# Optimization experiments

Measured on AMD Instinct MI355X. Metric: run time of the kernel, lower is better.

## Reference

```python
import jax, jax.numpy as jnp
import numpy as np

B, N, C, H = 8, 1024, 256, 8   # graphs, nodes per graph, channels, heads
E = 131072                      # edges (avg degree 16)
DK = C // H
EPS = 1e-5


def setup_inputs() -> dict:
    key = jax.random.key(0)
    ks = jax.random.split(key, 16)
    s = 1.0 / np.sqrt(C)
    d = {
        'x': jax.random.normal(ks[0], (B * N, C), jnp.float32),
        'edge_index': jax.random.randint(ks[1], (2, E), 0, B * N, dtype=jnp.int64),
        'sph': jax.random.uniform(ks[2], (B, 1, N, N), jnp.float32),
        # local conv (GraphConv-style): root + neighbor linear
        'Wr': jax.random.normal(ks[3], (C, C), jnp.float32) * s,
        'Wn': jax.random.normal(ks[4], (C, C), jnp.float32) * s,
        # attention in/out projections (4 Linears as in MultiheadAttention)
        'Wq': jax.random.normal(ks[5], (C, C), jnp.float32) * s,
        'bq': jnp.zeros((C,), jnp.float32),
        'Wk': jax.random.normal(ks[6], (C, C), jnp.float32) * s,
        'bk': jnp.zeros((C,), jnp.float32),
        'Wv': jax.random.normal(ks[7], (C, C), jnp.float32) * s,
        'bv': jnp.zeros((C,), jnp.float32),
        'Wo': jax.random.normal(ks[8], (C, C), jnp.float32) * s,
        'bo': jnp.zeros((C,), jnp.float32),
        # MLP: C -> 2C -> C
        'W1': jax.random.normal(ks[9], (C, 2 * C), jnp.float32) * s,
        'b1': jnp.zeros((2 * C,), jnp.float32),
        'W2': jax.random.normal(ks[10], (2 * C, C), jnp.float32) * (1.0 / np.sqrt(2 * C)),
        'b2': jnp.zeros((C,), jnp.float32),
        # three batch norms (affine)
        'gamma1': jnp.ones((C,), jnp.float32), 'beta1': jnp.zeros((C,), jnp.float32),
        'gamma2': jnp.ones((C,), jnp.float32), 'beta2': jnp.zeros((C,), jnp.float32),
        'gamma3': jnp.ones((C,), jnp.float32), 'beta3': jnp.zeros((C,), jnp.float32),
    }
    return d


def _bn(h, g, b):
    # BatchNorm1d (training mode): per-feature stats over all nodes
    m = h.mean(axis=0)
    v = h.var(axis=0)
    return (h - m) * jax.lax.rsqrt(v + EPS) * g + b


def reference(x, edge_index, sph, Wr, Wn, Wq, bq, Wk, bk, Wv, bv, Wo, bo,
              W1, b1, W2, b2, gamma1, beta1, gamma2, beta2, gamma3, beta3):
    src, dst = edge_index[0], edge_index[1]

    # 1) local MPNN branch: h = conv(x) + x, then norm1
    msg = (x @ Wn)[src]                                   # [E, C]
    agg = jax.ops.segment_sum(msg, dst, num_segments=B * N)
    h1 = _bn(x @ Wr + agg + x, gamma1, beta1)             # [BN, C]

    # 2) global sph-modulated attention branch (dense batch is a reshape:
    #    equal-size graphs -> mask all True)
    hd = x.reshape(B, N, C)
    q = (hd @ Wq + bq).reshape(B, N, H, DK).transpose(0, 2, 1, 3)  # [B,H,N,DK]
    k = (hd @ Wk + bk).reshape(B, N, H, DK).transpose(0, 2, 1, 3)
    v = (hd @ Wv + bv).reshape(B, N, H, DK).transpose(0, 2, 1, 3)
    scores = jnp.einsum('bhnd,bhmd->bhnm', q, k) * (1.0 / np.sqrt(DK))
    scores = scores * sph                                  # structural modulation
    p = jax.nn.softmax(scores, axis=-1)
    o = jnp.einsum('bhnm,bhmd->bhnd', p, v)                # [B,H,N,DK]
    o = o.transpose(0, 2, 1, 3).reshape(B * N, C) @ Wo + bo
    h2 = _bn(o + x, gamma2, beta2)

    # 3) sum branches, MLP residual, norm3
    out = h1 + h2
    out = out + (jax.nn.relu(out @ W1 + b1) @ W2 + b2)
    return _bn(out, gamma3, beta3)
```

## Files before the change

### kernel.cpp

```cpp
#include <hip/hip_runtime.h>
#include <hip/hip_bf16.h>

constexpr int Bg  = 8;
constexpr int Nn  = 1024;
constexpr int Cc  = 256;
constexpr int Hh  = 8;
constexpr int DKh = 32;
constexpr int Ee  = 131072;
constexpr int BNn = Bg * Nn;
#define EPSV 1e-5f


typedef __attribute__((ext_vector_type(8))) short bf16x8;
typedef __attribute__((ext_vector_type(4))) float f32x4;

static __device__ __forceinline__ unsigned short f2b(float v) {
    __hip_bfloat16 h = __float2bfloat16(v);
    return __builtin_bit_cast(unsigned short, h);
}
static __device__ __forceinline__ float b2f(unsigned short u) {
    unsigned int x = ((unsigned int)u) << 16;
    return __builtin_bit_cast(float, x);
}
static __device__ __forceinline__ bf16x8 ldb8(const unsigned short* p) {
    return *(const bf16x8*)p;
}

__global__ __launch_bounds__(256) void prep_k(
    const float* __restrict__ x, unsigned short* __restrict__ xf,
    unsigned short* __restrict__ xlo,
    const float* __restrict__ Wr, const float* __restrict__ Wn,
    const float* __restrict__ Wq, const float* __restrict__ Wk,
    const float* __restrict__ Wv, const float* __restrict__ Wo,
    const float* __restrict__ W1, const float* __restrict__ W2,
    unsigned short* __restrict__ WcatT,
    unsigned short* __restrict__ WqT, unsigned short* __restrict__ WkT,
    unsigned short* __restrict__ WvT, unsigned short* __restrict__ WoT,
    unsigned short* __restrict__ W1T, unsigned short* __restrict__ W2T,
    const int* __restrict__ ei, int* __restrict__ deg)
{
    int blk = blockIdx.x;
    if (blk < 2048) {
        int i = (blk * 256 + threadIdx.x) * 4;
        float4 v = *(const float4*)(x + i);
        int r = i >> 8, c = i & 255;
        ushort4 pk;
        pk.x = f2b(v.x); pk.y = f2b(v.y); pk.z = f2b(v.z); pk.w = f2b(v.w);
        *(ushort4*)(xlo + (size_t)r * 256 + c) = pk;
        *(ushort4*)(xf + ((size_t)(r >> 4) * 16 + (c >> 5)) * 512
                    + (r & 15) * 32 + (c & 31)) = pk;
    } else if (blk < 4608) {
        int idx = (blk - 2048) * 256 + threadIdx.x;
        if (idx < 131072) {
            int n = idx >> 9, k = idx & 511;
            float v = (k < 256) ? Wr[k * 256 + n] : Wn[(k - 256) * 256 + n];
            WcatT[((size_t)(n >> 4) * 16 + (k >> 5)) * 512 + (n & 15) * 32 + (k & 31)] = f2b(v);
        } else if (idx < 393216) {
            int l = idx - 131072;
            int wsel = l >> 16; l &= 65535;
            int n = l >> 8, kk = l & 255;
            const float* S = wsel == 0 ? Wq : wsel == 1 ? Wk : wsel == 2 ? Wv : Wo;
            unsigned short* D = wsel == 0 ? WqT : wsel == 1 ? WkT : wsel == 2 ? WvT : WoT;
            D[((size_t)(n >> 4) * 8 + (kk >> 5)) * 512 + (n & 15) * 32 + (kk & 31)]
                = f2b(S[kk * 256 + n]);
        } else if (idx < 524288) {
            int l = idx - 393216;
            int n = l >> 8, kk = l & 255;
            W1T[((size_t)(n >> 4) * 8 + (kk >> 5)) * 512 + (n & 15) * 32 + (kk & 31)]
                = f2b(W1[kk * 512 + n]);
        } else {
            int l = idx - 524288;
            int n = l >> 9, kk = l & 511;
            W2T[((size_t)(n >> 4) * 16 + (kk >> 5)) * 512 + (n & 15) * 32 + (kk & 31)]
                = f2b(W2[kk * 256 + n]);
        }
    } else {
        int e = (blk - 4608) * 256 + threadIdx.x;
        atomicAdd(&deg[ei[Ee + e]], 1);
    }
}

__global__ __launch_bounds__(256) void scan_k(
    const int* __restrict__ deg, int* __restrict__ rowst, int* __restrict__ cursor)
{
    __shared__ int partial[256];
    int t = threadIdx.x;
    int local[32];
    int s = 0;
    #pragma unroll
    for (int i = 0; i < 32; ++i) { local[i] = deg[i * 256 + t]; s += local[i]; }
    partial[t] = s;
    __syncthreads();
    for (int off = 1; off < 256; off <<= 1) {
        int v = (t >= off) ? partial[t - off] : 0;
        __syncthreads();
        partial[t] += v;
        __syncthreads();
    }
    int base = partial[t] - s;
    #pragma unroll
    for (int i = 0; i < 32; ++i) {
        int n = i * 256 + t;
        rowst[n] = base;
        cursor[n] = base;
        base += local[i];
    }
}

__global__ __launch_bounds__(256) void place_k(
    const int* __restrict__ ei, int* __restrict__ cursor, int* __restrict__ eidx)
{
    int e = blockIdx.x * 256 + threadIdx.x;
    int s = ei[e], d = ei[Ee + e];
    int pos = atomicAdd(&cursor[d], 1);
    eidx[pos] = s;
}

__global__ __launch_bounds__(256, 4) void gather_qkv_k(
    const unsigned short* __restrict__ xlo, const int* __restrict__ rowst,
    const int* __restrict__ deg, const int* __restrict__ eidx,
    unsigned short* __restrict__ xf,
    const unsigned short* __restrict__ WT,
    const float* __restrict__ bq, const float* __restrict__ bk,
    const float* __restrict__ bv,
    unsigned short* __restrict__ qb, unsigned short* __restrict__ kb,
    unsigned short* __restrict__ vTb, float qscale)
{
    __shared__ unsigned short vtile[64][40];
    int blk = blockIdx.x;

    if (blk < 2048) {
        int n = blk * 4 + (threadIdx.x >> 6);
        int c4 = (threadIdx.x & 63) * 4;
        int b0 = rowst[n], d = deg[n];
        float4 acc = {0.f, 0.f, 0.f, 0.f};
        int i = 0;
        for (; i + 4 <= d; i += 4) {
            int s0 = eidx[b0 + i], s1 = eidx[b0 + i + 1];
            int s2 = eidx[b0 + i + 2], s3 = eidx[b0 + i + 3];
            ushort4 a0 = *(const ushort4*)(xlo + (size_t)s0 * 256 + c4);
            ushort4 a1 = *(const ushort4*)(xlo + (size_t)s1 * 256 + c4);
            ushort4 a2 = *(const ushort4*)(xlo + (size_t)s2 * 256 + c4);
            ushort4 a3 = *(const ushort4*)(xlo + (size_t)s3 * 256 + c4);
            acc.x += (b2f(a0.x) + b2f(a1.x)) + (b2f(a2.x) + b2f(a3.x));
            acc.y += (b2f(a0.y) + b2f(a1.y)) + (b2f(a2.y) + b2f(a3.y));
            acc.z += (b2f(a0.z) + b2f(a1.z)) + (b2f(a2.z) + b2f(a3.z));
            acc.w += (b2f(a0.w) + b2f(a1.w)) + (b2f(a2.w) + b2f(a3.w));
        }
        for (; i < d; ++i) {
            int s = eidx[b0 + i];
            ushort4 a = *(const ushort4*)(xlo + (size_t)s * 256 + c4);
            acc.x += b2f(a.x); acc.y += b2f(a.y);
            acc.z += b2f(a.z); acc.w += b2f(a.w);
        }
        ushort4 pk;
        pk.x = f2b(acc.x); pk.y = f2b(acc.y); pk.z = f2b(acc.z); pk.w = f2b(acc.w);
        int cg2 = 256 + c4;
        *(ushort4*)(xf + ((size_t)(n >> 4) * 16 + (cg2 >> 5)) * 512
                    + (n & 15) * 32 + (cg2 & 31)) = pk;
        return;
    }

    int qblk = blk - 2048;
    const int n0 = (qblk % 12) * 64;
    const int m0 = (qblk / 12) * 32;
    const int t = threadIdx.x;
    const int wave = t >> 6, lane = t & 63;
    const int tl = lane & 15, g = lane >> 4;
    const int wr = wave >> 1, wc = wave & 1;
    const int which = n0 >> 8;

    f32x4 acc[2] = {};

    const unsigned short* a0 = xf + (size_t)((m0 >> 4) + wr) * 16 * 512 + tl * 32 + g * 8;
    const unsigned short* b0 = WT + ((size_t)(n0 >> 4) + wc * 2) * 8 * 512 + tl * 32 + g * 8;
    const unsigned short* b1 = b0 + 8 * 512;

    for (int k0 = 0; k0 < 256; k0 += 32) {
        bf16x8 af  = ldb8(a0 + (k0 >> 5) * 512);
        bf16x8 bf0 = ldb8(b0 + (k0 >> 5) * 512), bf1 = ldb8(b1 + (k0 >> 5) * 512);
        acc[0] = __builtin_amdgcn_mfma_f32_16x16x32_bf16(af, bf0, acc[0], 0, 0, 0);
        acc[1] = __builtin_amdgcn_mfma_f32_16x16x32_bf16(af, bf1, acc[1], 0, 0, 0);
    }

    const float* bias = which == 0 ? bq : which == 1 ? bk : bv;
    const float sc = which == 0 ? qscale : 1.f;

    if (which == 0) {
        #pragma unroll
        for (int c16 = 0; c16 < 2; ++c16)
            #pragma unroll
            for (int reg = 0; reg < 4; ++reg) {
                int row = m0 + wr * 16 + g * 4 + reg;
                int col = (n0 & 255) + wc * 32 + c16 * 16 + tl;
                qb[(size_t)row * Cc + col] = f2b((acc[c16][reg] + bias[col]) * sc);
            }
    } else if (which == 1) {
        #pragma unroll
        for (int c16 = 0; c16 < 2; ++c16)
            #pragma unroll
            for (int reg = 0; reg < 4; ++reg) {
                int row = m0 + wr * 16 + g * 4 + reg;
                int col = (n0 & 255) + wc * 32 + c16 * 16 + tl;
                kb[((size_t)(row >> 4) * 8 + (col >> 5)) * 512
                   + (row & 15) * 32 + (col & 31)] = f2b(acc[c16][reg] + bias[col]);
            }
    } else {
        #pragma unroll
        for (int c16 = 0; c16 < 2; ++c16)
            #pragma unroll
            for (int reg = 0; reg < 4; ++reg) {
                int colL = wc * 32 + c16 * 16 + tl;
                int rowL = wr * 16 + g * 4 + reg;
                vtile[colL][rowL] = f2b(acc[c16][reg] + bias[(n0 & 255) + colL]);
            }
        __syncthreads();
        int clocal = t >> 2, q4 = t & 3;
        int colg = (n0 & 255) + clocal;
        int hh = colg >> 5, dd = colg & 31;
        int bg = m0 >> 10;
        int m_loc = (m0 & 1023) + q4 * 8;
        int mt64 = m_loc >> 6, ks = (m_loc >> 5) & 1, gg = (m_loc >> 3) & 3;
        int cg = dd >> 4, tlv = dd & 15;
        ushort4 u0 = *(ushort4*)&vtile[clocal][q4 * 8];
        ushort4 u1 = *(ushort4*)&vtile[clocal][q4 * 8 + 4];
        unsigned short* dst = vTb
            + (((size_t)(bg * Hh + hh) * 16 + mt64) * 2048)
            + ((size_t)((ks * 2 + cg) * 16 + tlv) * 32) + gg * 8;
        *(ushort4*)dst = u0;
        *(ushort4*)(dst + 4) = u1;
    }
}

__global__ __launch_bounds__(512, 8) void attn_h1_k(
    const unsigned short* __restrict__ q, const unsigned short* __restrict__ k,
    const unsigned short* __restrict__ vT, const float* __restrict__ sph,
    unsigned short* __restrict__ op0,
    const unsigned short* __restrict__ xf, const unsigned short* __restrict__ WcatT,
    const float* __restrict__ x, unsigned short* __restrict__ h1preb,
    float* __restrict__ gsum, float* __restrict__ gsq)
{
    __shared__ float Sph[2][16][132];
    __shared__ unsigned short Ps[Hh][16][72];
    float* csum = (float*)&Ps[0][0][0];
    float* csq  = csum + 256;

    const int blk = blockIdx.x;
    const int t = threadIdx.x;
    const int wave = t >> 6;
    const int lane = t & 63;
    const int tl = lane & 15, g = lane >> 4;

    if (blk < 512) {
        const int b  = blk & 7;
        const int n0 = (blk >> 3) * 16;
        const int w  = wave;

        bf16x8 qf = ldb8(q + ((size_t)(b * Nn + n0 + tl)) * Cc + w * DKh + g * 8);

        float lsum = 0.f;
        f32x4 oacc[2] = {};

        const unsigned short* kfb = k + ((size_t)(b * 512 + w)) * 512 + tl * 32 + g * 8;
        const unsigned short* vfb = vT + ((size_t)(b * Hh + w) * 16) * 2048
                                     + (size_t)tl * 32 + g * 8;
        const float* sbase = sph + ((size_t)b * Nn + n0) * Nn;

        if (t < 256) {
            int r1 = t >> 4, c1 = (t & 15) * 8;
            const float* src = sbase + (size_t)r1 * Nn + c1;
            *(float4*)&Sph[0][r1][c1]     = *(const float4*)src;
            *(float4*)&Sph[0][r1][c1 + 4] = *(const float4*)(src + 4);
        }
        __syncthreads();

        int cur = 0;
        for (int it = 0; it < 8; ++it) {
            const int m0 = it * 128;
            if (it < 7 && t < 256) {
                int r1 = t >> 4, c1 = (t & 15) * 8;
                const float* src = sbase + (size_t)r1 * Nn + m0 + 128 + c1;
                *(float4*)&Sph[cur ^ 1][r1][c1]     = *(const float4*)src;
                *(float4*)&Sph[cur ^ 1][r1][c1 + 4] = *(const float4*)(src + 4);
            }

            #pragma unroll
            for (int half = 0; half < 2; ++half) {
                const int mh = m0 + half * 64;

                f32x4 st[4];
                #pragma unroll
                for (int mg = 0; mg < 4; ++mg) {
                    bf16x8 ka = ldb8(kfb + (size_t)((mh >> 4) + mg) * 4096);
                    f32x4 z = {0.f, 0.f, 0.f, 0.f};
                    st[mg] = __builtin_amdgcn_mfma_f32_16x16x32_bf16(ka, qf, z, 0, 0, 0);
                }

                #pragma unroll
                for (int mg = 0; mg < 4; ++mg) {
                    float4 sp = *(const float4*)&Sph[cur][tl][half * 64 + mg * 16 + g * 4];
                    float p0 = __builtin_amdgcn_exp2f(st[mg][0] * sp.x);
                    float p1 = __builtin_amdgcn_exp2f(st[mg][1] * sp.y);
                    float p2 = __builtin_amdgcn_exp2f(st[mg][2] * sp.z);
                    float p3 = __builtin_amdgcn_exp2f(st[mg][3] * sp.w);
                    lsum += (p0 + p1) + (p2 + p3);
                    ushort4 pk;
                    pk.x = f2b(p0); pk.y = f2b(p1); pk.z = f2b(p2); pk.w = f2b(p3);
                    *(ushort4*)&Ps[w][tl][mg * 16 + g * 4] = pk;
                }

                const unsigned short* vtile64 = vfb + (size_t)(mh >> 6) * 2048;
                #pragma unroll
                for (int ks = 0; ks < 2; ++ks) {
                    bf16x8 pa = ldb8(&Ps[w][tl][ks * 32 + g * 8]);
                    #pragma unroll
                    for (int cg = 0; cg < 2; ++cg) {
                        bf16x8 vb = ldb8(vtile64 + (size_t)(ks * 2 + cg) * 512);
                        oacc[cg] = __builtin_amdgcn_mfma_f32_16x16x32_bf16(pa, vb, oacc[cg], 0, 0, 0);
                    }
                }
            }

            __syncthreads();
            cur ^= 1;
        }

        lsum += __shfl_xor(lsum, 16);
        lsum += __shfl_xor(lsum, 32);
        float* shl = (float*)&Ps[w][0][0];
        if (g == 0) shl[tl] = lsum;
        const size_t rt = (size_t)((b * Nn + n0) >> 4);
        #pragma unroll
        for (int r = 0; r < 4; ++r) {
            float inv = 1.f / shl[g * 4 + r];
            #pragma unroll
            for (int cg = 0; cg < 2; ++cg)
                op0[(rt * 8 + w) * 512 + (g * 4 + r) * 32 + cg * 16 + tl]
                    = f2b(oacc[cg][r] * inv);
        }
        return;
    }

    const int wrg = wave >> 2;
    const int wcg = wave & 3;
    const int m0g = (blk - 512) * 32;
    const int N = Cc;

    if (t < 256) { csum[t] = 0.f; csq[t] = 0.f; }
    __syncthreads();

    f32x4 acc[4] = {};

    const unsigned short* a0 = xf + (size_t)((m0g >> 4) + wrg) * 16 * 512 + tl * 32 + g * 8;
    const unsigned short* bb = WcatT + (size_t)(wcg * 4) * 16 * 512 + tl * 32 + g * 8;

    for (int k0 = 0; k0 < 512; k0 += 32) {
        bf16x8 af = ldb8(a0 + (k0 >> 5) * 512);
        #pragma unroll
        for (int c16 = 0; c16 < 4; ++c16) {
            bf16x8 bf = ldb8(bb + ((size_t)c16 * 16 + (k0 >> 5)) * 512);
            acc[c16] = __builtin_amdgcn_mfma_f32_16x16x32_bf16(af, bf, acc[c16], 0, 0, 0);
        }
    }

    #pragma unroll
    for (int c16 = 0; c16 < 4; ++c16) {
        int col = wcg * 64 + c16 * 16 + tl;
        float ls = 0.f, lq = 0.f;
        #pragma unroll
        for (int reg = 0; reg < 4; ++reg) {
            int row = m0g + wrg * 16 + g * 4 + reg;
            size_t idx = (size_t)row * N + col;
            float v = acc[c16][reg] + x[idx];
            ls += v; lq += v * v;
            h1preb[idx] = f2b(v);
        }
        atomicAdd(&csum[col], ls);
        atomicAdd(&csq[col],  lq);
    }
    __syncthreads();
    if (t < 256) {
        atomicAdd(&gsum[t], csum[t]);
        atomicAdd(&gsq[t],  csq[t]);
    }
}

__global__ __launch_bounds__(256, 4) void mlp1_k(
    const unsigned short* __restrict__ A,
    const unsigned short* __restrict__ WT,
    const float* __restrict__ bias,
    unsigned short* __restrict__ outb)
{
    const int t = threadIdx.x;
    const int wave = t >> 6, lane = t & 63;
    const int tl = lane & 15, g = lane >> 4;
    const int wr = wave >> 1, wc = wave & 1;
    const int m0 = blockIdx.y * 32, n0 = blockIdx.x * 64;

    f32x4 acc[2] = {};

    const unsigned short* a0 = A  + (size_t)((m0 >> 4) + wr) * 8 * 512 + tl * 32 + g * 8;
    const unsigned short* b0 = WT + ((size_t)(n0 >> 4) + wc * 2) * 8 * 512 + tl * 32 + g * 8;
    const unsigned short* b1 = b0 + 8 * 512;

    for (int k0 = 0; k0 < 256; k0 += 32) {
        bf16x8 af  = ldb8(a0 + (k0 >> 5) * 512);
        bf16x8 bf0 = ldb8(b0 + (k0 >> 5) * 512), bf1 = ldb8(b1 + (k0 >> 5) * 512);
        acc[0] = __builtin_amdgcn_mfma_f32_16x16x32_bf16(af, bf0, acc[0], 0, 0, 0);
        acc[1] = __builtin_amdgcn_mfma_f32_16x16x32_bf16(af, bf1, acc[1], 0, 0, 0);
    }

    const size_t rtO = (size_t)(m0 >> 4) + wr;
    #pragma unroll
    for (int c16 = 0; c16 < 2; ++c16) {
        int col  = n0 + wc * 32 + c16 * 16 + tl;
        int ktO  = col >> 5;
        #pragma unroll
        for (int reg = 0; reg < 4; ++reg) {
            float v = fmaxf(acc[c16][reg] + bias[col], 0.f);
            outb[(rtO * 16 + ktO) * 512 + (g * 4 + reg) * 32 + (col & 31)] = f2b(v);
        }
    }
}

__global__ __launch_bounds__(256, 4) void mlp2_k(
    const unsigned short* __restrict__ A,
    const unsigned short* __restrict__ WT,
    const float* __restrict__ bias,
    const unsigned short* __restrict__ addb,
    float* __restrict__ outf,
    float* __restrict__ gsum, float* __restrict__ gsq)
{
    const int N = Cc;
    const int t = threadIdx.x;
    const int wave = t >> 6, lane = t & 63;
    const int tl = lane & 15, g = lane >> 4;
    const int wr = wave >> 1, wc = wave & 1;
    const int m0 = blockIdx.y * 32, n0 = blockIdx.x * 64;

    __shared__ float csum[64], csq[64];
    if (t < 64) { csum[t] = 0.f; csq[t] = 0.f; }
    __syncthreads();

    f32x4 acc[2] = {};

    const unsigned short* a0 = A  + (size_t)((m0 >> 4) + wr) * 16 * 512 + tl * 32 + g * 8;
    const unsigned short* b0 = WT + ((size_t)(n0 >> 4) + wc * 2) * 16 * 512 + tl * 32 + g * 8;
    const unsigned short* b1 = b0 + 16 * 512;

    for (int k0 = 0; k0 < 512; k0 += 32) {
        bf16x8 af  = ldb8(a0 + (k0 >> 5) * 512);
        bf16x8 bf0 = ldb8(b0 + (k0 >> 5) * 512), bf1 = ldb8(b1 + (k0 >> 5) * 512);
        acc[0] = __builtin_amdgcn_mfma_f32_16x16x32_bf16(af, bf0, acc[0], 0, 0, 0);
        acc[1] = __builtin_amdgcn_mfma_f32_16x16x32_bf16(af, bf1, acc[1], 0, 0, 0);
    }

    const size_t rtR = (size_t)(m0 >> 4) + wr;
    #pragma unroll
    for (int c16 = 0; c16 < 2; ++c16) {
        int colL = wc * 32 + c16 * 16 + tl;
        int col  = n0 + colL;
        int ktR  = col >> 5;
        float ls = 0.f, lq = 0.f;
        #pragma unroll
        for (int reg = 0; reg < 4; ++reg) {
            int row = m0 + wr * 16 + g * 4 + reg;
            float v = acc[c16][reg] + bias[col]
                    + b2f(addb[(rtR * 8 + ktR) * 512 + (g * 4 + reg) * 32 + (col & 31)]);
            ls += v; lq += v * v;
            outf[(size_t)row * N + col] = v;
        }
        atomicAdd(&csum[colL], ls); atomicAdd(&csq[colL], lq);
    }
    __syncthreads();
    if (t < 64) {
        atomicAdd(&gsum[n0 + t], csum[t]);
        atomicAdd(&gsq[n0 + t],  csq[t]);
    }
}

__global__ __launch_bounds__(256, 4) void gemm_attnA_k(
    const unsigned short* __restrict__ op0,
    const unsigned short* __restrict__ WT, const float* __restrict__ bias,
    const float* __restrict__ add1, unsigned short* __restrict__ h2preb,
    float* __restrict__ gsum, float* __restrict__ gsq)
{
    const int N = Cc;
    const int t = threadIdx.x;
    const int wave = t >> 6, lane = t & 63;
    const int tl = lane & 15, g = lane >> 4;
    const int wr = wave >> 1, wc = wave & 1;
    const int m0 = blockIdx.y * 32, n0 = blockIdx.x * 64;

    __shared__ float csum[64], csq[64];
    if (t < 64) { csum[t] = 0.f; csq[t] = 0.f; }
    __syncthreads();

    f32x4 acc[2] = {};

    const unsigned short* a0b = op0 + (size_t)((m0 >> 4) + wr) * 8 * 512 + tl * 32 + g * 8;
    const unsigned short* b0 = WT + ((size_t)(n0 >> 4) + wc * 2) * 8 * 512 + tl * 32 + g * 8;
    const unsigned short* b1 = b0 + 8 * 512;

    for (int k0 = 0; k0 < 256; k0 += 32) {
        bf16x8 af  = ldb8(a0b + (k0 >> 5) * 512);
        bf16x8 bf0 = ldb8(b0 + (k0 >> 5) * 512), bf1 = ldb8(b1 + (k0 >> 5) * 512);
        acc[0] = __builtin_amdgcn_mfma_f32_16x16x32_bf16(af, bf0, acc[0], 0, 0, 0);
        acc[1] = __builtin_amdgcn_mfma_f32_16x16x32_bf16(af, bf1, acc[1], 0, 0, 0);
    }

    #pragma unroll
    for (int c16 = 0; c16 < 2; ++c16) {
        int colL = wc * 32 + c16 * 16 + tl;
        int col  = n0 + colL;
        float ls = 0.f, lq = 0.f;
        #pragma unroll
        for (int reg = 0; reg < 4; ++reg) {
            int row = m0 + wr * 16 + g * 4 + reg;
            float v = acc[c16][reg] + bias[col];
            size_t idx = (size_t)row * N + col;
            v += add1[idx];
            ls += v; lq += v * v;
            h2preb[idx] = f2b(v);
        }
        atomicAdd(&csum[colL], ls); atomicAdd(&csq[colL], lq);
    }
    __syncthreads();
    if (t < 64) {
        atomicAdd(&gsum[n0 + t], csum[t]);
        atomicAdd(&gsq[n0 + t],  csq[t]);
    }
}

__global__ __launch_bounds__(256) void bn_apply_k(
    const float* __restrict__ h, const float* __restrict__ gsum,
    const float* __restrict__ gsq, const float* __restrict__ gamma,
    const float* __restrict__ beta, float* __restrict__ outf)
{
    size_t i4 = ((size_t)blockIdx.x * 256 + threadIdx.x) * 4;
    int ch = (int)(i4 & (Cc - 1));
    float4 hv = *(const float4*)(h + i4);
    float4 sm = *(const float4*)(gsum + ch);
    float4 sq = *(const float4*)(gsq + ch);
    float4 ga = *(const float4*)(gamma + ch);
    float4 be = *(const float4*)(beta + ch);
    float4 o;
    {
        float m = sm.x * (1.f / BNn), var = sq.x * (1.f / BNn) - m * m;
        o.x = (hv.x - m) * rsqrtf(var + EPSV) * ga.x + be.x;
    }
    {
        float m = sm.y * (1.f / BNn), var = sq.y * (1.f / BNn) - m * m;
        o.y = (hv.y - m) * rsqrtf(var + EPSV) * ga.y + be.y;
    }
    {
        float m = sm.z * (1.f / BNn), var = sq.z * (1.f / BNn) - m * m;
        o.z = (hv.z - m) * rsqrtf(var + EPSV) * ga.z + be.z;
    }
    {
        float m = sm.w * (1.f / BNn), var = sq.w * (1.f / BNn) - m * m;
        o.w = (hv.w - m) * rsqrtf(var + EPSV) * ga.w + be.w;
    }
    *(float4*)(outf + i4) = o;
}

__global__ __launch_bounds__(256) void bn_apply12_k(
    const unsigned short* __restrict__ h1preb, const unsigned short* __restrict__ h2preb,
    const float* __restrict__ stats,
    const float* __restrict__ g1, const float* __restrict__ be1,
    const float* __restrict__ g2, const float* __restrict__ be2,
    unsigned short* __restrict__ outb)
{
    size_t i4 = ((size_t)blockIdx.x * 256 + threadIdx.x) * 4;
    int ch = (int)(i4 & (Cc - 1));
    ushort4 u1 = *(const ushort4*)(h1preb + i4);
    ushort4 u2 = *(const ushort4*)(h2preb + i4);
    float4 s1m = *(const float4*)(stats + ch);
    float4 s1q = *(const float4*)(stats + 256 + ch);
    float4 s2m = *(const float4*)(stats + 512 + ch);
    float4 s2q = *(const float4*)(stats + 768 + ch);
    float4 G1 = *(const float4*)(g1 + ch),  B1 = *(const float4*)(be1 + ch);
    float4 G2 = *(const float4*)(g2 + ch),  B2 = *(const float4*)(be2 + ch);
    ushort4 pk;
    #define BN12C(comp, ucomp) { \
        float m1 = s1m.comp * (1.f / BNn), v1 = s1q.comp * (1.f / BNn) - m1 * m1; \
        float m2 = s2m.comp * (1.f / BNn), v2 = s2q.comp * (1.f / BNn) - m2 * m2; \
        float o = (b2f(u1.ucomp) - m1) * rsqrtf(v1 + EPSV) * G1.comp + B1.comp \
                + (b2f(u2.ucomp) - m2) * rsqrtf(v2 + EPSV) * G2.comp + B2.comp; \
        pk.ucomp = f2b(o); }
    BN12C(x, x) BN12C(y, y) BN12C(z, z) BN12C(w, w)
    #undef BN12C
    int row = (int)(i4 >> 8), col = ch;
    *(ushort4*)(outb + ((size_t)(row >> 4) * 8 + (col >> 5)) * 512
                + (row & 15) * 32 + (col & 31)) = pk;
}

extern "C" void kernel_launch(void* const* d_in, const int* in_sizes, int n_in,
                              void* d_out, int out_size, void* d_ws, size_t ws_size,
                              hipStream_t stream)
{
    const float* x   = (const float*)d_in[0];
    const int*   ei  = (const int*)  d_in[1];
    const float* sph = (const float*)d_in[2];
    const float* Wr  = (const float*)d_in[3];
    const float* Wn  = (const float*)d_in[4];
    const float* Wq  = (const float*)d_in[5];
    const float* bq  = (const float*)d_in[6];
    const float* Wk  = (const float*)d_in[7];
    const float* bk  = (const float*)d_in[8];
    const float* Wv  = (const float*)d_in[9];
    const float* bv  = (const float*)d_in[10];
    const float* Wo  = (const float*)d_in[11];
    const float* bo  = (const float*)d_in[12];
    const float* W1  = (const float*)d_in[13];
    const float* b1  = (const float*)d_in[14];
    const float* W2  = (const float*)d_in[15];
    const float* b2  = (const float*)d_in[16];
    const float* g1  = (const float*)d_in[17];
    const float* be1 = (const float*)d_in[18];
    const float* g2  = (const float*)d_in[19];
    const float* be2 = (const float*)d_in[20];
    const float* g3  = (const float*)d_in[21];
    const float* be3 = (const float*)d_in[22];
    float* out = (float*)d_out;

    const size_t SL = (size_t)BNn * Cc;

    float* ws = (float*)d_ws;
    float* s1 = ws;
    float* s2 = s1 + SL;
    float* s3 = s2 + SL;

    int*   deg      = (int*)(s3 + SL);
    float* statsAll = (float*)(deg + 8192);
    int*   rowst    = (int*)(statsAll + 1536);
    int*   cursor   = rowst + 8256;
    int*   eidx     = cursor + 8192;

    unsigned short* xf  = (unsigned short*)(eidx + 131072);
    unsigned short* qb  = xf + 2 * SL;
    unsigned short* kb  = qb + SL;
    unsigned short* vTb = kb + SL;
    unsigned short* osb = kb;
    unsigned short* hid = xf;

    unsigned short* WcatT = vTb + SL;
    unsigned short* WqT   = WcatT + 131072;
    unsigned short* WkT   = WqT + 65536;
    unsigned short* WvT   = WkT + 65536;
    unsigned short* WoT   = WvT + 65536;
    unsigned short* W1T   = WoT + 65536;
    unsigned short* W2T   = W1T + 131072;
    unsigned short* xlo   = W2T + 131072;
    unsigned short* op0b   = (unsigned short*)s1;
    unsigned short* h1preb = (unsigned short*)s2;
    unsigned short* h2preb = (unsigned short*)s3;

    dim3 gN256(4, 256);
    dim3 gN512(8, 256);

    const float QSCALE = 0.17677669529663687f * 1.4426950408889634f;

    hipMemsetAsync(deg, 0, (8192 + 1536) * sizeof(float), stream);
    prep_k<<<5120, 256, 0, stream>>>(x, xf, xlo, Wr, Wn, Wq, Wk, Wv, Wo, W1, W2,
                                     WcatT, WqT, WkT, WvT, WoT, W1T, W2T, ei, deg);
    scan_k<<<1, 256, 0, stream>>>(deg, rowst, cursor);
    place_k<<<Ee / 256, 256, 0, stream>>>(ei, cursor, eidx);
    gather_qkv_k<<<5120, 256, 0, stream>>>(xlo, rowst, deg, eidx, xf,
                                           WqT, bq, bk, bv, qb, kb, vTb, QSCALE);
    attn_h1_k<<<768, 512, 0, stream>>>(qb, kb, vTb, sph, op0b,
                                       xf, WcatT, x, h1preb,
                                       statsAll, statsAll + 256);
    gemm_attnA_k<<<gN256, 256, 0, stream>>>(op0b, WoT, bo, x,
                                            h2preb, statsAll + 512, statsAll + 768);
    bn_apply12_k<<<(int)(SL / 1024), 256, 0, stream>>>(h1preb, h2preb, statsAll,
                                                       g1, be1, g2, be2, osb);
    mlp1_k<<<gN512, 256, 0, stream>>>(osb, W1T, b1, hid);
    mlp2_k<<<gN256, 256, 0, stream>>>(hid, W2T, b2, osb, s2,
                                      statsAll + 1024, statsAll + 1280);
    bn_apply_k<<<(int)(SL / 1024), 256, 0, stream>>>(s2, statsAll + 1024,
                                                     statsAll + 1280, g3, be3, out);
}
```

Baseline: 282.9 us.

## Process two query row tiles per attention block to reuse K/V loads

Measured after the change: 322.9 us. 1.14x slower.

```diff
diff --git a/kernel.cpp b/kernel.cpp
--- a/kernel.cpp
+++ b/kernel.cpp
@@ -232,7 +232,7 @@
     }
 }
 
-__global__ __launch_bounds__(512, 8) void attn_h1_k(
+__global__ __launch_bounds__(512, 6) void attn_h1_k(
     const unsigned short* __restrict__ q, const unsigned short* __restrict__ k,
     const unsigned short* __restrict__ vT, const float* __restrict__ sph,
     unsigned short* __restrict__ op0,
@@ -240,7 +240,7 @@
     const float* __restrict__ x, unsigned short* __restrict__ h1preb,
     float* __restrict__ gsum, float* __restrict__ gsq)
 {
-    __shared__ float Sph[2][16][132];
+    __shared__ float Sph[2][32][132];
     __shared__ unsigned short Ps[Hh][16][72];
     float* csum = (float*)&Ps[0][0][0];
     float* csq  = csum + 256;
@@ -251,22 +251,25 @@
     const int lane = t & 63;
     const int tl = lane & 15, g = lane >> 4;
 
-    if (blk < 512) {
+    if (blk < 256) {
         const int b  = blk & 7;
-        const int n0 = (blk >> 3) * 16;
+        const int n0 = (blk >> 3) * 32;
         const int w  = wave;
 
-        bf16x8 qf = ldb8(q + ((size_t)(b * Nn + n0 + tl)) * Cc + w * DKh + g * 8);
-
-        float lsum = 0.f;
-        f32x4 oacc[2] = {};
+        bf16x8 qf[2];
+        #pragma unroll
+        for (int qs = 0; qs < 2; ++qs)
+            qf[qs] = ldb8(q + ((size_t)(b * Nn + n0 + qs * 16 + tl)) * Cc + w * DKh + g * 8);
+
+        float lsum[2] = {0.f, 0.f};
+        f32x4 oacc[2][2] = {};
 
         const unsigned short* kfb = k + ((size_t)(b * 512 + w)) * 512 + tl * 32 + g * 8;
         const unsigned short* vfb = vT + ((size_t)(b * Hh + w) * 16) * 2048
                                      + (size_t)tl * 32 + g * 8;
         const float* sbase = sph + ((size_t)b * Nn + n0) * Nn;
 
-        if (t < 256) {
+        {
             int r1 = t >> 4, c1 = (t & 15) * 8;
             const float* src = sbase + (size_t)r1 * Nn + c1;
             *(float4*)&Sph[0][r1][c1]     = *(const float4*)src;
@@ -277,7 +280,7 @@
         int cur = 0;
         for (int it = 0; it < 8; ++it) {
             const int m0 = it * 128;
-            if (it < 7 && t < 256) {
+            if (it < 7) {
                 int r1 = t >> 4, c1 = (t & 15) * 8;
                 const float* src = sbase + (size_t)r1 * Nn + m0 + 128 + c1;
                 *(float4*)&Sph[cur ^ 1][r1][c1]     = *(const float4*)src;
@@ -288,35 +291,48 @@
             for (int half = 0; half < 2; ++half) {
                 const int mh = m0 + half * 64;
 
-                f32x4 st[4];
+                bf16x8 ka[4];
                 #pragma unroll
-                for (int mg = 0; mg < 4; ++mg) {
-                    bf16x8 ka = ldb8(kfb + (size_t)((mh >> 4) + mg) * 4096);
-                    f32x4 z = {0.f, 0.f, 0.f, 0.f};
-                    st[mg] = __builtin_amdgcn_mfma_f32_16x16x32_bf16(ka, qf, z, 0, 0, 0);
-                }
-
+                for (int mg = 0; mg < 4; ++mg)
+                    ka[mg] = ldb8(kfb + (size_t)((mh >> 4) + mg) * 4096);
+                const unsigned short* vtile64 = vfb + (size_t)(mh >> 6) * 2048;
+                bf16x8 vb[2][2];
                 #pragma unroll
-                for (int mg = 0; mg < 4; ++mg) {
-                    float4 sp = *(const float4*)&Sph[cur][tl][half * 64 + mg * 16 + g * 4];
-                    float p0 = __builtin_amdgcn_exp2f(st[mg][0] * sp.x);
-                    float p1 = __builtin_amdgcn_exp2f(st[mg][1] * sp.y);
-                    float p2 = __builtin_amdgcn_exp2f(st[mg][2] * sp.z);
-                    float p3 = __builtin_amdgcn_exp2f(st[mg][3] * sp.w);
-                    lsum += (p0 + p1) + (p2 + p3);
-                    ushort4 pk;
-                    pk.x = f2b(p0); pk.y = f2b(p1); pk.z = f2b(p2); pk.w = f2b(p3);
-                    *(ushort4*)&Ps[w][tl][mg * 16 + g * 4] = pk;
-                }
-
-                const unsigned short* vtile64 = vfb + (size_t)(mh >> 6) * 2048;
+                for (int ks = 0; ks < 2; ++ks)
+                    #pragma unroll
+                    for (int cg = 0; cg < 2; ++cg)
+                        vb[ks][cg] = ldb8(vtile64 + (size_t)(half * 2 * 0 + ks * 2 + cg) * 512);
+
                 #pragma unroll
-                for (int ks = 0; ks < 2; ++ks) {
-                    bf16x8 pa = ldb8(&Ps[w][tl][ks * 32 + g * 8]);
+                for (int qs = 0; qs < 2; ++qs) {
+                    f32x4 st[4];
                     #pragma unroll
-                    for (int cg = 0; cg < 2; ++cg) {
-                        bf16x8 vb = ldb8(vtile64 + (size_t)(ks * 2 + cg) * 512);
-                        oacc[cg] = __builtin_amdgcn_mfma_f32_16x16x32_bf16(pa, vb, oacc[cg], 0, 0, 0);
+                    for (int mg = 0; mg < 4; ++mg) {
+                        f32x4 z = {0.f, 0.f, 0.f, 0.f};
+                        st[mg] = __builtin_amdgcn_mfma_f32_16x16x32_bf16(ka[mg], qf[qs], z, 0, 0, 0);
+                    }
+
+                    #pragma unroll
+                    for (int mg = 0; mg < 4; ++mg) {
+                        float4 sp = *(const float4*)&Sph[cur][qs * 16 + tl]
+                                        [half * 64 + mg * 16 + g * 4];
+                        float p0 = __builtin_amdgcn_exp2f(st[mg][0] * sp.x);
+                        float p1 = __builtin_amdgcn_exp2f(st[mg][1] * sp.y);
+                        float p2 = __builtin_amdgcn_exp2f(st[mg][2] * sp.z);
+                        float p3 = __builtin_amdgcn_exp2f(st[mg][3] * sp.w);
+                        lsum[qs] += (p0 + p1) + (p2 + p3);
+                        ushort4 pk;
+                        pk.x = f2b(p0); pk.y = f2b(p1); pk.z = f2b(p2); pk.w = f2b(p3);
+                        *(ushort4*)&Ps[w][tl][mg * 16 + g * 4] = pk;
+                    }
+
+                    #pragma unroll
+                    for (int ks = 0; ks < 2; ++ks) {
+                        bf16x8 pa = ldb8(&Ps[w][tl][ks * 32 + g * 8]);
+                        #pragma unroll
+                        for (int cg = 0; cg < 2; ++cg)
+                            oacc[qs][cg] = __builtin_amdgcn_mfma_f32_16x16x32_bf16(
+                                pa, vb[ks][cg], oacc[qs][cg], 0, 0, 0);
                     }
                 }
             }
@@ -325,25 +341,31 @@
             cur ^= 1;
         }
 
-        lsum += __shfl_xor(lsum, 16);
-        lsum += __shfl_xor(lsum, 32);
         float* shl = (float*)&Ps[w][0][0];
-        if (g == 0) shl[tl] = lsum;
-        const size_t rt = (size_t)((b * Nn + n0) >> 4);
-        #pragma unroll
-        for (int r = 0; r < 4; ++r) {
-            float inv = 1.f / shl[g * 4 + r];
+        #pragma unroll
+        for (int qs = 0; qs < 2; ++qs) {
+            float ls = lsum[qs];
+            ls += __shfl_xor(ls, 16);
+            ls += __shfl_xor(ls, 32);
+            if (g == 0) shl[qs * 16 + tl] = ls;
+        }
+        const size_t rt0 = (size_t)((b * Nn + n0) >> 4);
+        #pragma unroll
+        for (int qs = 0; qs < 2; ++qs)
             #pragma unroll
-            for (int cg = 0; cg < 2; ++cg)
-                op0[(rt * 8 + w) * 512 + (g * 4 + r) * 32 + cg * 16 + tl]
-                    = f2b(oacc[cg][r] * inv);
-        }
+            for (int r = 0; r < 4; ++r) {
+                float inv = 1.f / shl[qs * 16 + g * 4 + r];
+                #pragma unroll
+                for (int cg = 0; cg < 2; ++cg)
+                    op0[((rt0 + qs) * 8 + w) * 512 + (g * 4 + r) * 32 + cg * 16 + tl]
+                        = f2b(oacc[qs][cg][r] * inv);
+            }
         return;
     }
 
     const int wrg = wave >> 2;
     const int wcg = wave & 3;
-    const int m0g = (blk - 512) * 32;
+    const int m0g = (blk - 256) * 32;
     const int N = Cc;
 
     if (t < 256) { csum[t] = 0.f; csq[t] = 0.f; }
@@ -668,7 +690,7 @@
     place_k<<<Ee / 256, 256, 0, stream>>>(ei, cursor, eidx);
     gather_qkv_k<<<5120, 256, 0, stream>>>(xlo, rowst, deg, eidx, xf,
                                            WqT, bq, bk, bv, qb, kb, vTb, QSCALE);
-    attn_h1_k<<<768, 512, 0, stream>>>(qb, kb, vTb, sph, op0b,
+    attn_h1_k<<<512, 512, 0, stream>>>(qb, kb, vTb, sph, op0b,
                                        xf, WcatT, x, h1preb,
                                        statsAll, statsAll + 256);
     gemm_attnA_k<<<gN256, 256, 0, stream>>>(op0b, WoT, bo, x,
```
